# Optimization experiments

Hardware: AMD Instinct MI355X
Metric: run time of the kernel (lower is better)

Reference implementation:

```python
import jax, jax.numpy as jnp
import numpy as np

K = 3        # kernel_size
PAD = 1      # padding
STRIDE = 1   # stride


def conv2d(x, w, stride, pad):
    return jax.lax.conv_general_dilated(
        x, w, (stride, stride), [(pad, pad), (pad, pad)],
        dimension_numbers=('NCHW', 'OIHW', 'NCHW'))


def setup_inputs() -> dict:
    key = jax.random.key(0)
    ks = jax.random.split(key, 6)
    B, C, H, W, O = 8, 64, 64, 64, 128
    N = K * K
    x = jax.random.normal(ks[0], (B, C, H, W), jnp.float32)
    # offset (shift) conv: 2N output channels; small weights so sampled
    # positions deviate a few pixels from the regular grid
    shift_w = jax.random.normal(ks[1], (2 * N, C, 3, 3), jnp.float32) * 0.01
    shift_b = jax.random.normal(ks[2], (2 * N,), jnp.float32) * 0.5
    # modulation conv: N output channels
    mod_w = jax.random.normal(ks[3], (N, C, 3, 3), jnp.float32) * 0.01
    mod_b = jax.random.normal(ks[4], (N,), jnp.float32) * 0.1
    # final conv (bias=False), applied with stride=K on the unfolded map
    conv_w = jax.random.normal(ks[5], (O, C, K, K), jnp.float32) / np.sqrt(C * K * K)
    return {'x': x, 'shift_w': shift_w, 'shift_b': shift_b,
            'mod_w': mod_w, 'mod_b': mod_b, 'conv_w': conv_w}


def reference(x, shift_w, shift_b, mod_w, mod_b, conv_w):
    B, C, H, W = x.shape
    k = conv_w.shape[-1]
    N = k * k
    # offsets and modulation from 3x3 convs on the raw input
    offset = conv2d(x, shift_w, STRIDE, 1) + shift_b[None, :, None, None]   # (B,2N,H,W)
    modulation = jax.nn.sigmoid(conv2d(x, mod_w, STRIDE, 1) + mod_b[None, :, None, None])  # (B,N,H,W)

    xp = jnp.pad(x, ((0, 0), (0, 0), (PAD, PAD), (PAD, PAD)))  # zero padding
    Hp, Wp = xp.shape[2], xp.shape[3]

    # p_n: kernel-relative offsets, ij meshgrid, x-block then y-block -> (2N,)
    r = (k - 1) // 2
    pn_x, pn_y = jnp.meshgrid(jnp.arange(-r, r + 1), jnp.arange(-r, r + 1), indexing='ij')
    pn = jnp.concatenate([pn_x.ravel(), pn_y.ravel()]).astype(x.dtype)
    # p_0: base grid starts at 1 (accounts for padding)
    p0x = jnp.broadcast_to(jnp.arange(1, H * STRIDE + 1, STRIDE, dtype=x.dtype)[:, None], (H, W))
    p0y = jnp.broadcast_to(jnp.arange(1, W * STRIDE + 1, STRIDE, dtype=x.dtype)[None, :], (H, W))
    p0 = jnp.concatenate([jnp.broadcast_to(p0x, (N, H, W)),
                          jnp.broadcast_to(p0y, (N, H, W))], 0)  # (2N,H,W)

    pos = offset + pn[None, :, None, None] + p0[None]            # (B,2N,H,W)
    pos = jnp.transpose(pos, (0, 2, 3, 1))                       # (B,H,W,2N)
    px, py = pos[..., :N], pos[..., N:]

    # NOTE: original clamps to output H/W (not padded dims) -- kept faithfully
    fx, fy = jnp.floor(px), jnp.floor(py)
    lt_x = jnp.clip(fx, 0, H - 1).astype(jnp.int32)
    lt_y = jnp.clip(fy, 0, W - 1).astype(jnp.int32)
    rb_x = jnp.clip(fx + 1, 0, H - 1).astype(jnp.int32)
    rb_y = jnp.clip(fy + 1, 0, W - 1).astype(jnp.int32)
    # original casts clamped position to long -> integer bilinear weights
    p_x = jnp.clip(px, 0, H - 1).astype(jnp.int32)
    p_y = jnp.clip(py, 0, W - 1).astype(jnp.int32)

    g_lt = ((1 + (lt_x - p_x)) * (1 + (lt_y - p_y))).astype(x.dtype)
    g_rb = ((1 - (rb_x - p_x)) * (1 - (rb_y - p_y))).astype(x.dtype)
    g_lb = ((1 + (lt_x - p_x)) * (1 + (rb_y - p_y))).astype(x.dtype)  # lb=(lt_x,rb_y)
    g_rt = ((1 - (rb_x - p_x)) * (1 - (lt_y - p_y))).astype(x.dtype)  # rt=(rb_x,lt_y)

    x_flat = xp.reshape(B, C, Hp * Wp)

    def gather(qx, qy):
        idx = (qx * Wp + qy).reshape(B, 1, -1)                     # (B,1,H*W*N)
        v = jnp.take_along_axis(x_flat, jnp.broadcast_to(idx, (B, C, idx.shape[-1])), axis=-1)
        return v.reshape(B, C, H, W, N)

    x_off = (g_lt[:, None] * gather(lt_x, lt_y)
             + g_rb[:, None] * gather(rb_x, rb_y)
             + g_lb[:, None] * gather(lt_x, rb_y)
             + g_rt[:, None] * gather(rb_x, lt_y))                 # (B,C,H,W,N)

    mod = jnp.transpose(modulation, (0, 2, 3, 1))[:, None]        # (B,1,H,W,N)
    x_off = x_off * mod

    # unfold: out[h*k+a, w*k+b] = x_off[h, w, a*k+b]
    x_off = x_off.reshape(B, C, H, W, k, k).transpose(0, 1, 2, 4, 3, 5).reshape(B, C, H * k, W * k)
    return conv2d(x_off, conv_w, k, 0)                            # (B,O,H,W)
```

## Files before the change

### kernel.cpp

```cpp
#include <hip/hip_runtime.h>
#include <hip/hip_fp16.h>
#include <math.h>


typedef _Float16 half8_t __attribute__((ext_vector_type(8)));
typedef float f32x4 __attribute__((ext_vector_type(4)));

__global__ __launch_bounds__(256) void k_pre(const float* __restrict__ x,
                                             const float* __restrict__ cw,
                                             const float* __restrict__ shift_w,
                                             const float* __restrict__ mod_w,
                                             __half* __restrict__ xTh,
                                             __half* __restrict__ xTl,
                                             __half* __restrict__ xCb,
                                             __half* __restrict__ WtF,
                                             __half* __restrict__ WtSFh,
                                             __half* __restrict__ WtSFl) {
    __shared__ float tile[64][65];
    int bid = blockIdx.x;
    int t = threadIdx.x;
    if (bid < 512) {
        int b = bid >> 6, pt = bid & 63;
        int lane = t & 63, cq = t >> 6;
        const float* xb = x + ((size_t)b << 18);
#pragma unroll
        for (int r = 0; r < 16; ++r) {
            int c = cq * 16 + r;
            tile[c][lane] = xb[((size_t)c << 12) + pt * 64 + lane];
        }
        __syncthreads();
        int p = t >> 2, qc = t & 3;
        __align__(16) _Float16 hh[16];
        __align__(16) _Float16 ll[16];
        __align__(16) _Float16 cb[16];
#pragma unroll
        for (int k = 0; k < 16; ++k) {
            float v0 = tile[qc * 16 + k][p];
            float v1 = (p < 63) ? tile[qc * 16 + k][p + 1] : 0.f;
            _Float16 h = (_Float16)v0;
            hh[k] = h;
            ll[k] = (_Float16)(v0 - (float)h);
            cb[k] = (_Float16)(v0 + 2.f * v1);
        }
        size_t off = ((size_t)b << 18) + (size_t)(pt * 64 + p) * 64 + qc * 16;
        ((uint4*)(xTh + off))[0] = ((uint4*)hh)[0];
        ((uint4*)(xTh + off))[1] = ((uint4*)hh)[1];
        ((uint4*)(xTl + off))[0] = ((uint4*)ll)[0];
        ((uint4*)(xTl + off))[1] = ((uint4*)ll)[1];
        ((uint4*)(xCb + off))[0] = ((uint4*)cb)[0];
        ((uint4*)(xCb + off))[1] = ((uint4*)cb)[1];
    } else {
        int u = (bid - 512) * 256 + t;
        if (u < 73728) {
            int e = u & 7, l = (u >> 3) & 63, ks = (u >> 9) & 1;
            int g = (u >> 10) & 3, w = (u >> 12) & 1, n = u >> 13;
            int o = w * 64 + g * 16 + (l & 15);
            int c = ks * 32 + (l >> 4) * 8 + e;
            WtF[u] = __float2half_rn(cw[(o * 64 + c) * 9 + n]);
        } else {
            int q = u - 73728;
            if (q < 18432) {
                int e = q & 7, l = (q >> 3) & 63, nf = (q >> 9) & 1;
                int chf = (q >> 10) & 1, tap = q >> 11;
                int ch = nf * 16 + (l & 15);
                int c = chf * 32 + (l >> 4) * 8 + e;
                float wv = 0.f;
                if (ch < 18) wv = shift_w[(ch * 64 + c) * 9 + tap];
                else if (ch < 27) wv = mod_w[((ch - 18) * 64 + c) * 9 + tap];
                _Float16 h = (_Float16)wv;
                _Float16 lo = (_Float16)(wv - (float)h);
                WtSFh[q] = *(__half*)&h;
                WtSFl[q] = *(__half*)&lo;
            }
        }
    }
}

__global__ __launch_bounds__(512, 2) void k_fused(
    const __half* __restrict__ xTh, const __half* __restrict__ xTl,
    const __half* __restrict__ xCb, const __half* __restrict__ WtF,
    const __half* __restrict__ WtSFh, const __half* __restrict__ WtSFl,
    const float* __restrict__ shift_b, const float* __restrict__ mod_b,
    float* __restrict__ out) {
    __shared__ __align__(16) unsigned char arena[50688];
    __shared__ float Cw[2][4][16][36];
    __shared__ uint4 recA[9][64];

    int t = threadIdx.x;
    int l = t & 63;
    int w = t >> 6;
    int l15 = l & 15, lhi = l >> 4;

    int bid = blockIdx.x;
    int bk = (bid & 7) * 64 + (bid >> 3);
    int b = bk >> 6;
    int row = bk & 63;

    const __half* xbh = xTh + ((size_t)b << 18);
    const __half* xbl = xTl + ((size_t)b << 18);
    const __half* xbc = xCb + ((size_t)b << 18);

#pragma unroll
    for (int rr = 0; rr < 7; ++rr) {
        int d = rr * 512 + t;
        if (d < 3168) {
            int bufl = d >= 1584 ? 1 : 0;
            int dd = d - bufl * 1584;
            int s = dd >> 3, cb8 = dd & 7;
            int r = s / 66, j = s - r * 66;
            int grow = row + r - 1;
            int gcol = j - 1;
            uint4 v = make_uint4(0u, 0u, 0u, 0u);
            if ((unsigned)grow < 64u && (unsigned)gcol < 64u) {
                const __half* src = (bufl ? xbl : xbh) +
                                    ((size_t)((grow << 6) + gcol) << 6) + (cb8 << 3);
                v = *(const uint4*)src;
            }
            int dst = bufl * 25344 + s * 128 + ((cb8 << 4) ^ ((s & 7) << 4));
            *(uint4*)&arena[dst] = v;
        }
    }
    __syncthreads();

    {
        int wp = w >> 1, wh = w & 1;
        f32x4 accA[2];
        accA[0] = (f32x4){0.f, 0.f, 0.f, 0.f};
        accA[1] = (f32x4){0.f, 0.f, 0.f, 0.f};
#pragma unroll
        for (int tr = 0; tr < 3; ++tr)
#pragma unroll
            for (int tc = 0; tc < 3; ++tc) {
                int tap = tr * 3 + tc;
                int j = wp * 16 + l15 + tc;
                int s = tr * 66 + j;
                int cbyte = (wh << 6) + (lhi << 4);
                int addr = s * 128 + (cbyte ^ ((s & 7) << 4));
                half8_t Ah = *(const half8_t*)&arena[addr];
                half8_t Al = *(const half8_t*)&arena[25344 + addr];
#pragma unroll
                for (int nf = 0; nf < 2; ++nf) {
                    int fo = ((((tap << 1) + wh) << 1) + nf) << 9;
                    half8_t Bh = *(const half8_t*)(WtSFh + fo + (l << 3));
                    half8_t Bl = *(const half8_t*)(WtSFl + fo + (l << 3));
                    accA[nf] = __builtin_amdgcn_mfma_f32_16x16x32_f16(Ah, Bh, accA[nf], 0, 0, 0);
                    accA[nf] = __builtin_amdgcn_mfma_f32_16x16x32_f16(Ah, Bl, accA[nf], 0, 0, 0);
                    accA[nf] = __builtin_amdgcn_mfma_f32_16x16x32_f16(Al, Bh, accA[nf], 0, 0, 0);
                }
            }
#pragma unroll
        for (int nf = 0; nf < 2; ++nf)
#pragma unroll
            for (int v4 = 0; v4 < 4; ++v4)
                Cw[wh][wp][(lhi << 2) + v4][nf * 16 + l15] = accA[nf][v4];
    }
    __syncthreads();

#pragma unroll
    for (int jj0 = 0; jj0 < 2; ++jj0) {
        int rid = jj0 * 512 + t;
        if (rid < 576) {
            int p = rid & 63;
            int n = rid >> 6;
            int wp = p >> 4, pp = p & 15;
            float sx = Cw[0][wp][pp][n] + Cw[1][wp][pp][n];
            float sy = Cw[0][wp][pp][9 + n] + Cw[1][wp][pp][9 + n];
            float sm = Cw[0][wp][pp][18 + n] + Cw[1][wp][pp][18 + n];

            float px = ((sx + shift_b[n]) + (float)(n / 3 - 1)) + (float)(row + 1);
            float py = ((sy + shift_b[9 + n]) + (float)(n % 3 - 1)) + (float)(p + 1);
            float mod = 1.f / (1.f + expf(-(sm + mod_b[n])));

            float fx = floorf(px), fy = floorf(py);
            int ltx = (int)fminf(fmaxf(fx, 0.f), 63.f);
            int lty = (int)fminf(fmaxf(fy, 0.f), 63.f);
            int rbx = (int)fminf(fmaxf(fx + 1.f, 0.f), 63.f);
            int rby = (int)fminf(fmaxf(fy + 1.f, 0.f), 63.f);
            int pxi = (int)fminf(fmaxf(px, 0.f), 63.f);
            int pyi = (int)fminf(fmaxf(py, 0.f), 63.f);

            int g_lt = (1 + ltx - pxi) * (1 + lty - pyi);
            int g_rb = (1 - rbx + pxi) * (1 - rby + pyi);
            int g_lb = (1 + ltx - pxi) * (1 + rby - pyi);
            int g_rt = (1 - rbx + pxi) * (1 - lty + pyi);

            bool simple = (ltx == pxi) && (lty == pyi) && (rbx == pxi + 1) &&
                          (rby == pyi + 1) && (ltx >= 1) && (lty >= 1);

            int qxa[4] = {ltx, rbx, ltx, rbx};
            int qya[4] = {lty, rby, rby, lty};
            int gga[4] = {g_lt, g_rb, g_lb, g_rt};
            unsigned w0 = 0, w1 = 0;
#pragma unroll
            for (int jq = 0; jq < 4; ++jq) {
                bool valid = (qxa[jq] >= 1) && (qya[jq] >= 1);
                unsigned idx = valid ? (unsigned)((qxa[jq] - 1) * 64 + (qya[jq] - 1)) : 0u;
                unsigned gc = valid ? (unsigned)gga[jq] : 0u;
                if (jq < 2) w0 |= idx << (12 * jq); else w1 |= idx << (12 * (jq - 2));
                w0 |= gc << (24 + 2 * jq);
            }
            if (simple) w1 |= 0x80000000u;
            recA[n][p] = make_uint4(w0, w1, __float_as_uint(mod), 0u);
        }
    }
    __syncthreads();

    int wm = w >> 1, wn = w & 1;
    int mA = t >> 3, cg = t & 7;

    f32x4 acc[4];
#pragma unroll
    for (int g = 0; g < 4; ++g) acc[g] = (f32x4){0.f, 0.f, 0.f, 0.f};

    for (int n = 0; n < 9; ++n) {
        int sl = n & 1;
        {
            const uint4* wsrc = (const uint4*)(WtF + n * 8192);
            uint4* wdst = (uint4*)&arena[16384 + (sl << 14)];
            wdst[t] = wsrc[t];
            wdst[512 + t] = wsrc[512 + t];
        }

        {
            uint4 rc = recA[n][mA];
            float mod = __uint_as_float(rc.z);
            __align__(16) __half2 a2[4];
            if (rc.y >> 31) {
                int idx = (int)(rc.x & 0xFFF);
                uint4 v = *(const uint4*)(xbc + (idx << 6) + (cg << 3));
                __half mh = __float2half_rn(mod);
                __half2 mm(mh, mh);
                const __half2* vv = (const __half2*)&v;
                a2[0] = __hmul2(mm, vv[0]);
                a2[1] = __hmul2(mm, vv[1]);
                a2[2] = __hmul2(mm, vv[2]);
                a2[3] = __hmul2(mm, vv[3]);
            } else {
                a2[0] = __half2(0, 0); a2[1] = __half2(0, 0);
                a2[2] = __half2(0, 0); a2[3] = __half2(0, 0);
#pragma unroll
                for (int jq = 0; jq < 4; ++jq) {
                    int id = (int)((jq < 2 ? (rc.x >> (12 * jq))
                                           : (rc.y >> (12 * (jq - 2)))) & 0xFFF);
                    float wf = (float)((rc.x >> (24 + 2 * jq)) & 3) * mod;
                    __half2 wh2 = __half2(__float2half_rn(wf), __float2half_rn(wf));
                    uint4 v = *(const uint4*)(xbh + (id << 6) + (cg << 3));
                    const __half2* vv = (const __half2*)&v;
                    a2[0] = __hfma2(wh2, vv[0], a2[0]);
                    a2[1] = __hfma2(wh2, vv[1], a2[1]);
                    a2[2] = __hfma2(wh2, vv[2], a2[2]);
                    a2[3] = __hfma2(wh2, vv[3], a2[3]);
                }
            }
            *(uint4*)&arena[(sl << 13) | (mA << 7) | ((cg ^ (mA & 7)) << 4)] =
                *(uint4*)a2;
        }
        __syncthreads();

        const unsigned char* wsl = &arena[16384 + (sl << 14)];
#pragma unroll
        for (int ks = 0; ks < 2; ++ks) {
            int rowa = wm * 16 + l15;
            int gr = (ks * 4 + lhi) ^ (rowa & 7);
            half8_t Af = *(const half8_t*)&arena[(sl << 13) | (rowa << 7) | (gr << 4)];
#pragma unroll
            for (int g = 0; g < 4; ++g) {
                half8_t Bf = *(const half8_t*)&wsl[((((wn << 2) + g) << 1) + ks) * 1024 +
                                                   (l << 4)];
                acc[g] = __builtin_amdgcn_mfma_f32_16x16x32_f16(Af, Bf, acc[g], 0, 0, 0);
            }
        }
    }

    __syncthreads();
    float* Ep = (float*)arena;
#pragma unroll
    for (int g = 0; g < 4; ++g) {
        int o_loc = (wn << 6) + (g << 4) + l15;
#pragma unroll
        for (int v4 = 0; v4 < 4; ++v4)
            Ep[o_loc * 65 + (wm << 4) + (lhi << 2) + v4] = acc[g][v4];
    }
    __syncthreads();
    {
        float* ob = out + ((size_t)b << 19);
        int prow = row << 6;
#pragma unroll
        for (int r = 0; r < 4; ++r) {
            int o_loc = (r << 5) + (t >> 4);
            int mseg = t & 15;
            float4 fa;
            fa.x = Ep[o_loc * 65 + mseg * 4 + 0];
            fa.y = Ep[o_loc * 65 + mseg * 4 + 1];
            fa.z = Ep[o_loc * 65 + mseg * 4 + 2];
            fa.w = Ep[o_loc * 65 + mseg * 4 + 3];
            float* dst = ob + (((size_t)o_loc) << 12) + prow + mseg * 4;
            *(float4*)dst = fa;
        }
    }
}

extern "C" void kernel_launch(void* const* d_in, const int* in_sizes, int n_in,
                              void* d_out, int out_size, void* d_ws, size_t ws_size,
                              hipStream_t stream) {
    const float* x = (const float*)d_in[0];
    const float* shift_w = (const float*)d_in[1];
    const float* shift_b = (const float*)d_in[2];
    const float* mod_w = (const float*)d_in[3];
    const float* mod_b = (const float*)d_in[4];
    const float* conv_w = (const float*)d_in[5];
    float* out = (float*)d_out;

    char* ws = (char*)d_ws;
    __half* xTh = (__half*)ws;
    __half* xTl = (__half*)(ws + 4194304);
    __half* xCb = (__half*)(ws + 8388608);
    __half* WtF = (__half*)(ws + 12582912);
    __half* WtSFh = (__half*)(ws + 12730368);
    __half* WtSFl = (__half*)(ws + 12767232);

    k_pre<<<dim3(872), dim3(256), 0, stream>>>(x, conv_w, shift_w, mod_w,
                                               xTh, xTl, xCb, WtF, WtSFh, WtSFl);
    k_fused<<<dim3(512), dim3(512), 0, stream>>>(xTh, xTl, xCb, WtF, WtSFh,
                                                 WtSFl, shift_b, mod_b, out);
}
```

Before: 36.45 us.

## Software-pipeline weight and gather loads ahead of MFMA in main loop

Restructures the 9-tap loop into a prologue plus a pipelined body. The next tap's weights and gathered input values are loaded into registers before the current tap's MFMAs are issued, then written to the alternate LDS slot afterwards. This hides global and gather latency behind matrix compute and needs only one barrier per iteration. The cost is more live registers, which may lower occupancy.

```diff
diff --git a/kernel.cpp b/kernel.cpp
--- a/kernel.cpp
+++ b/kernel.cpp
@@ -212,25 +212,96 @@
 #pragma unroll
     for (int g = 0; g < 4; ++g) acc[g] = (f32x4){0.f, 0.f, 0.f, 0.f};
 
+    {
+        const uint4* wsrc = (const uint4*)WtF;
+        uint4* wdst = (uint4*)&arena[16384];
+        wdst[t] = wsrc[t];
+        wdst[512 + t] = wsrc[512 + t];
+
+        uint4 rc = recA[0][mA];
+        float mod = __uint_as_float(rc.z);
+        __align__(16) __half2 a2[4];
+        if (rc.y >> 31) {
+            int idx = (int)(rc.x & 0xFFF);
+            uint4 v = *(const uint4*)(xbc + (idx << 6) + (cg << 3));
+            __half mh = __float2half_rn(mod);
+            __half2 mm(mh, mh);
+            const __half2* vv = (const __half2*)&v;
+            a2[0] = __hmul2(mm, vv[0]);
+            a2[1] = __hmul2(mm, vv[1]);
+            a2[2] = __hmul2(mm, vv[2]);
+            a2[3] = __hmul2(mm, vv[3]);
+        } else {
+            a2[0] = __half2(0, 0); a2[1] = __half2(0, 0);
+            a2[2] = __half2(0, 0); a2[3] = __half2(0, 0);
+#pragma unroll
+            for (int jq = 0; jq < 4; ++jq) {
+                int id = (int)((jq < 2 ? (rc.x >> (12 * jq))
+                                       : (rc.y >> (12 * (jq - 2)))) & 0xFFF);
+                float wf = (float)((rc.x >> (24 + 2 * jq)) & 3) * mod;
+                __half2 wh2 = __half2(__float2half_rn(wf), __float2half_rn(wf));
+                uint4 v = *(const uint4*)(xbh + (id << 6) + (cg << 3));
+                const __half2* vv = (const __half2*)&v;
+                a2[0] = __hfma2(wh2, vv[0], a2[0]);
+                a2[1] = __hfma2(wh2, vv[1], a2[1]);
+                a2[2] = __hfma2(wh2, vv[2], a2[2]);
+                a2[3] = __hfma2(wh2, vv[3], a2[3]);
+            }
+        }
+        *(uint4*)&arena[(mA << 7) | ((cg ^ (mA & 7)) << 4)] = *(uint4*)a2;
+    }
+    __syncthreads();
+
     for (int n = 0; n < 9; ++n) {
         int sl = n & 1;
+
+        uint4 wv0, wv1, rcN;
+        uint4 gr0, gr1, gr2, gr3;
+        bool simpleN = false;
+        if (n < 8) {
+            const uint4* wsrc = (const uint4*)(WtF + (n + 1) * 8192);
+            wv0 = wsrc[t];
+            wv1 = wsrc[512 + t];
+            rcN = recA[n + 1][mA];
+            simpleN = (rcN.y >> 31) != 0u;
+            if (simpleN) {
+                gr0 = *(const uint4*)(xbc + ((int)(rcN.x & 0xFFF) << 6) + (cg << 3));
+            } else {
+                gr0 = *(const uint4*)(xbh + ((int)(rcN.x & 0xFFF) << 6) + (cg << 3));
+                gr1 = *(const uint4*)(xbh + ((int)((rcN.x >> 12) & 0xFFF) << 6) + (cg << 3));
+                gr2 = *(const uint4*)(xbh + ((int)(rcN.y & 0xFFF) << 6) + (cg << 3));
+                gr3 = *(const uint4*)(xbh + ((int)((rcN.y >> 12) & 0xFFF) << 6) + (cg << 3));
+            }
+        }
+
         {
-            const uint4* wsrc = (const uint4*)(WtF + n * 8192);
-            uint4* wdst = (uint4*)&arena[16384 + (sl << 14)];
-            wdst[t] = wsrc[t];
-            wdst[512 + t] = wsrc[512 + t];
-        }
-
-        {
-            uint4 rc = recA[n][mA];
-            float mod = __uint_as_float(rc.z);
+            const unsigned char* wsl = &arena[16384 + (sl << 14)];
+#pragma unroll
+            for (int ks = 0; ks < 2; ++ks) {
+                int rowa = wm * 16 + l15;
+                int gr = (ks * 4 + lhi) ^ (rowa & 7);
+                half8_t Af = *(const half8_t*)&arena[(sl << 13) | (rowa << 7) | (gr << 4)];
+#pragma unroll
+                for (int g = 0; g < 4; ++g) {
+                    half8_t Bf = *(const half8_t*)&wsl[((((wn << 2) + g) << 1) + ks) * 1024 +
+                                                       (l << 4)];
+                    acc[g] = __builtin_amdgcn_mfma_f32_16x16x32_f16(Af, Bf, acc[g], 0, 0, 0);
+                }
+            }
+        }
+
+        if (n < 8) {
+            int s2 = sl ^ 1;
+            uint4* wdst = (uint4*)&arena[16384 + (s2 << 14)];
+            wdst[t] = wv0;
+            wdst[512 + t] = wv1;
+
+            float mod = __uint_as_float(rcN.z);
             __align__(16) __half2 a2[4];
-            if (rc.y >> 31) {
-                int idx = (int)(rc.x & 0xFFF);
-                uint4 v = *(const uint4*)(xbc + (idx << 6) + (cg << 3));
+            if (simpleN) {
                 __half mh = __float2half_rn(mod);
                 __half2 mm(mh, mh);
-                const __half2* vv = (const __half2*)&v;
+                const __half2* vv = (const __half2*)&gr0;
                 a2[0] = __hmul2(mm, vv[0]);
                 a2[1] = __hmul2(mm, vv[1]);
                 a2[2] = __hmul2(mm, vv[2]);
@@ -238,41 +309,24 @@
             } else {
                 a2[0] = __half2(0, 0); a2[1] = __half2(0, 0);
                 a2[2] = __half2(0, 0); a2[3] = __half2(0, 0);
+                const uint4* grs[4] = {&gr0, &gr1, &gr2, &gr3};
 #pragma unroll
                 for (int jq = 0; jq < 4; ++jq) {
-                    int id = (int)((jq < 2 ? (rc.x >> (12 * jq))
-                                           : (rc.y >> (12 * (jq - 2)))) & 0xFFF);
-                    float wf = (float)((rc.x >> (24 + 2 * jq)) & 3) * mod;
+                    float wf = (float)((rcN.x >> (24 + 2 * jq)) & 3) * mod;
                     __half2 wh2 = __half2(__float2half_rn(wf), __float2half_rn(wf));
-                    uint4 v = *(const uint4*)(xbh + (id << 6) + (cg << 3));
-                    const __half2* vv = (const __half2*)&v;
+                    const __half2* vv = (const __half2*)grs[jq];
                     a2[0] = __hfma2(wh2, vv[0], a2[0]);
                     a2[1] = __hfma2(wh2, vv[1], a2[1]);
                     a2[2] = __hfma2(wh2, vv[2], a2[2]);
                     a2[3] = __hfma2(wh2, vv[3], a2[3]);
                 }
             }
-            *(uint4*)&arena[(sl << 13) | (mA << 7) | ((cg ^ (mA & 7)) << 4)] =
+            *(uint4*)&arena[(s2 << 13) | (mA << 7) | ((cg ^ (mA & 7)) << 4)] =
                 *(uint4*)a2;
         }
         __syncthreads();
-
-        const unsigned char* wsl = &arena[16384 + (sl << 14)];
-#pragma unroll
-        for (int ks = 0; ks < 2; ++ks) {
-            int rowa = wm * 16 + l15;
-            int gr = (ks * 4 + lhi) ^ (rowa & 7);
-            half8_t Af = *(const half8_t*)&arena[(sl << 13) | (rowa << 7) | (gr << 4)];
-#pragma unroll
-            for (int g = 0; g < 4; ++g) {
-                half8_t Bf = *(const half8_t*)&wsl[((((wn << 2) + g) << 1) + ks) * 1024 +
-                                                   (l << 4)];
-                acc[g] = __builtin_amdgcn_mfma_f32_16x16x32_f16(Af, Bf, acc[g], 0, 0, 0);
-            }
-        }
-    }
-
-    __syncthreads();
+    }
+
     float* Ep = (float*)arena;
 #pragma unroll
     for (int g = 0; g < 4; ++g) {
```

Result: faster. 34.85 us (-4.4%).

## Software-pipeline gather and weight loads two stages ahead in fused deformable conv

Applied to the files above, without the earlier changes.

Restructures the main tap loop to issue global gathers and weight loads two iterations ahead into registers, writing the next LDS slab after the MFMA compute of the current slab, with one barrier per iteration instead of an implicit load-then-compute serialization. Also splits the offset-conv MFMA accumulation into three independent accumulators to break the dependency chain. Raises launch bounds to 4 blocks per SM-equivalent, which forces a lower register budget while the prefetch buffers add register pressure, risking spills. The goal is to hide global gather latency behind matrix math.

```diff
diff --git a/kernel.cpp b/kernel.cpp
--- a/kernel.cpp
+++ b/kernel.cpp
@@ -76,7 +76,36 @@
     }
 }
 
-__global__ __launch_bounds__(512, 2) void k_fused(
+__device__ __forceinline__ void combine_frag(uint4 rc, bool simple, float mod,
+                                             const uint4& g0, const uint4& g1,
+                                             const uint4& g2, const uint4& g3,
+                                             __half2* a2) {
+    if (simple) {
+        __half mh = __float2half_rn(mod);
+        __half2 mm(mh, mh);
+        const __half2* vv = (const __half2*)&g0;
+        a2[0] = __hmul2(mm, vv[0]);
+        a2[1] = __hmul2(mm, vv[1]);
+        a2[2] = __hmul2(mm, vv[2]);
+        a2[3] = __hmul2(mm, vv[3]);
+    } else {
+        a2[0] = __half2(0, 0); a2[1] = __half2(0, 0);
+        a2[2] = __half2(0, 0); a2[3] = __half2(0, 0);
+        const uint4* grs[4] = {&g0, &g1, &g2, &g3};
+#pragma unroll
+        for (int jq = 0; jq < 4; ++jq) {
+            float wf = (float)((rc.x >> (24 + 2 * jq)) & 3) * mod;
+            __half2 wh2 = __half2(__float2half_rn(wf), __float2half_rn(wf));
+            const __half2* vv = (const __half2*)grs[jq];
+            a2[0] = __hfma2(wh2, vv[0], a2[0]);
+            a2[1] = __hfma2(wh2, vv[1], a2[1]);
+            a2[2] = __hfma2(wh2, vv[2], a2[2]);
+            a2[3] = __hfma2(wh2, vv[3], a2[3]);
+        }
+    }
+}
+
+__global__ __launch_bounds__(512, 4) void k_fused(
     const __half* __restrict__ xTh, const __half* __restrict__ xTl,
     const __half* __restrict__ xCb, const __half* __restrict__ WtF,
     const __half* __restrict__ WtSFh, const __half* __restrict__ WtSFl,
@@ -124,9 +153,13 @@
 
     {
         int wp = w >> 1, wh = w & 1;
-        f32x4 accA[2];
-        accA[0] = (f32x4){0.f, 0.f, 0.f, 0.f};
-        accA[1] = (f32x4){0.f, 0.f, 0.f, 0.f};
+        f32x4 aP[2], aQ[2], aR[2];
+#pragma unroll
+        for (int nf = 0; nf < 2; ++nf) {
+            aP[nf] = (f32x4){0.f, 0.f, 0.f, 0.f};
+            aQ[nf] = (f32x4){0.f, 0.f, 0.f, 0.f};
+            aR[nf] = (f32x4){0.f, 0.f, 0.f, 0.f};
+        }
 #pragma unroll
         for (int tr = 0; tr < 3; ++tr)
 #pragma unroll
@@ -143,16 +176,17 @@
                     int fo = ((((tap << 1) + wh) << 1) + nf) << 9;
                     half8_t Bh = *(const half8_t*)(WtSFh + fo + (l << 3));
                     half8_t Bl = *(const half8_t*)(WtSFl + fo + (l << 3));
-                    accA[nf] = __builtin_amdgcn_mfma_f32_16x16x32_f16(Ah, Bh, accA[nf], 0, 0, 0);
-                    accA[nf] = __builtin_amdgcn_mfma_f32_16x16x32_f16(Ah, Bl, accA[nf], 0, 0, 0);
-                    accA[nf] = __builtin_amdgcn_mfma_f32_16x16x32_f16(Al, Bh, accA[nf], 0, 0, 0);
+                    aP[nf] = __builtin_amdgcn_mfma_f32_16x16x32_f16(Ah, Bh, aP[nf], 0, 0, 0);
+                    aQ[nf] = __builtin_amdgcn_mfma_f32_16x16x32_f16(Ah, Bl, aQ[nf], 0, 0, 0);
+                    aR[nf] = __builtin_amdgcn_mfma_f32_16x16x32_f16(Al, Bh, aR[nf], 0, 0, 0);
                 }
             }
 #pragma unroll
         for (int nf = 0; nf < 2; ++nf)
 #pragma unroll
             for (int v4 = 0; v4 < 4; ++v4)
-                Cw[wh][wp][(lhi << 2) + v4][nf * 16 + l15] = accA[nf][v4];
+                Cw[wh][wp][(lhi << 2) + v4][nf * 16 + l15] =
+                    (aP[nf][v4] + aQ[nf][v4]) + aR[nf][v4];
     }
     __syncthreads();
 
@@ -212,67 +246,80 @@
 #pragma unroll
     for (int g = 0; g < 4; ++g) acc[g] = (f32x4){0.f, 0.f, 0.f, 0.f};
 
+#define ISSUE(W0, W1, RC, SMP, G0, G1, G2, G3, nn)                             \
+    {                                                                          \
+        const uint4* wsrc_ = (const uint4*)(WtF + (nn) * 8192);                \
+        W0 = wsrc_[t];                                                         \
+        W1 = wsrc_[512 + t];                                                   \
+        RC = recA[nn][mA];                                                     \
+        SMP = (RC.y >> 31) != 0u;                                              \
+        if (SMP) {                                                             \
+            G0 = *(const uint4*)(xbc + ((int)(RC.x & 0xFFF) << 6) + (cg << 3));\
+        } else {                                                               \
+            G0 = *(const uint4*)(xbh + ((int)(RC.x & 0xFFF) << 6) + (cg << 3));\
+            G1 = *(const uint4*)(xbh + ((int)((RC.x >> 12) & 0xFFF) << 6) + (cg << 3)); \
+            G2 = *(const uint4*)(xbh + ((int)(RC.y & 0xFFF) << 6) + (cg << 3));\
+            G3 = *(const uint4*)(xbh + ((int)((RC.y >> 12) & 0xFFF) << 6) + (cg << 3)); \
+        }                                                                      \
+    }
+
+#define WRITE_SLAB(W0, W1, RC, SMP, G0, G1, G2, G3, slot)                      \
+    {                                                                          \
+        uint4* wdst_ = (uint4*)&arena[16384 + ((slot) << 14)];                 \
+        wdst_[t] = W0;                                                         \
+        wdst_[512 + t] = W1;                                                   \
+        __align__(16) __half2 a2_[4];                                          \
+        combine_frag(RC, SMP, __uint_as_float(RC.z), G0, G1, G2, G3, a2_);     \
+        *(uint4*)&arena[((slot) << 13) | (mA << 7) | ((cg ^ (mA & 7)) << 4)] = \
+            *(uint4*)a2_;                                                      \
+    }
+
+    uint4 wA0, wA1, rcA_, gA0, gA1, gA2, gA3;
+    uint4 wB0, wB1, rcB_, gB0, gB1, gB2, gB3;
+    bool smA = false, smB = false;
+
+    ISSUE(wA0, wA1, rcA_, smA, gA0, gA1, gA2, gA3, 0);
+    WRITE_SLAB(wA0, wA1, rcA_, smA, gA0, gA1, gA2, gA3, 0);
+    ISSUE(wA0, wA1, rcA_, smA, gA0, gA1, gA2, gA3, 1);
+    __syncthreads();
+
+#pragma unroll
     for (int n = 0; n < 9; ++n) {
         int sl = n & 1;
+
+        if (n < 7) {
+            ISSUE(wB0, wB1, rcB_, smB, gB0, gB1, gB2, gB3, n + 2);
+        }
+
         {
-            const uint4* wsrc = (const uint4*)(WtF + n * 8192);
-            uint4* wdst = (uint4*)&arena[16384 + (sl << 14)];
-            wdst[t] = wsrc[t];
-            wdst[512 + t] = wsrc[512 + t];
-        }
-
-        {
-            uint4 rc = recA[n][mA];
-            float mod = __uint_as_float(rc.z);
-            __align__(16) __half2 a2[4];
-            if (rc.y >> 31) {
-                int idx = (int)(rc.x & 0xFFF);
-                uint4 v = *(const uint4*)(xbc + (idx << 6) + (cg << 3));
-                __half mh = __float2half_rn(mod);
-                __half2 mm(mh, mh);
-                const __half2* vv = (const __half2*)&v;
-                a2[0] = __hmul2(mm, vv[0]);
-                a2[1] = __hmul2(mm, vv[1]);
-                a2[2] = __hmul2(mm, vv[2]);
-                a2[3] = __hmul2(mm, vv[3]);
-            } else {
-                a2[0] = __half2(0, 0); a2[1] = __half2(0, 0);
-                a2[2] = __half2(0, 0); a2[3] = __half2(0, 0);
-#pragma unroll
-                for (int jq = 0; jq < 4; ++jq) {
-                    int id = (int)((jq < 2 ? (rc.x >> (12 * jq))
-                                           : (rc.y >> (12 * (jq - 2)))) & 0xFFF);
-                    float wf = (float)((rc.x >> (24 + 2 * jq)) & 3) * mod;
-                    __half2 wh2 = __half2(__float2half_rn(wf), __float2half_rn(wf));
-                    uint4 v = *(const uint4*)(xbh + (id << 6) + (cg << 3));
-                    const __half2* vv = (const __half2*)&v;
-                    a2[0] = __hfma2(wh2, vv[0], a2[0]);
-                    a2[1] = __hfma2(wh2, vv[1], a2[1]);
-                    a2[2] = __hfma2(wh2, vv[2], a2[2]);
-                    a2[3] = __hfma2(wh2, vv[3], a2[3]);
+            const unsigned char* wsl = &arena[16384 + (sl << 14)];
+#pragma unroll
+            for (int ks = 0; ks < 2; ++ks) {
+                int rowa = wm * 16 + l15;
+                int gr = (ks * 4 + lhi) ^ (rowa & 7);
+                half8_t Af = *(const half8_t*)&arena[(sl << 13) | (rowa << 7) | (gr << 4)];
+#pragma unroll
+                for (int g = 0; g < 4; ++g) {
+                    half8_t Bf = *(const half8_t*)&wsl[((((wn << 2) + g) << 1) + ks) * 1024 +
+                                                       (l << 4)];
+                    acc[g] = __builtin_amdgcn_mfma_f32_16x16x32_f16(Af, Bf, acc[g], 0, 0, 0);
                 }
             }
-            *(uint4*)&arena[(sl << 13) | (mA << 7) | ((cg ^ (mA & 7)) << 4)] =
-                *(uint4*)a2;
+        }
+
+        if (n < 8) {
+            WRITE_SLAB(wA0, wA1, rcA_, smA, gA0, gA1, gA2, gA3, sl ^ 1);
+        }
+
+        if (n < 7) {
+            wA0 = wB0; wA1 = wB1; rcA_ = rcB_; smA = smB;
+            gA0 = gB0; gA1 = gB1; gA2 = gB2; gA3 = gB3;
         }
         __syncthreads();
-
-        const unsigned char* wsl = &arena[16384 + (sl << 14)];
-#pragma unroll
-        for (int ks = 0; ks < 2; ++ks) {
-            int rowa = wm * 16 + l15;
-            int gr = (ks * 4 + lhi) ^ (rowa & 7);
-            half8_t Af = *(const half8_t*)&arena[(sl << 13) | (rowa << 7) | (gr << 4)];
-#pragma unroll
-            for (int g = 0; g < 4; ++g) {
-                half8_t Bf = *(const half8_t*)&wsl[((((wn << 2) + g) << 1) + ks) * 1024 +
-                                                   (l << 4)];
-                acc[g] = __builtin_amdgcn_mfma_f32_16x16x32_f16(Af, Bf, acc[g], 0, 0, 0);
-            }
-        }
-    }
-
-    __syncthreads();
+    }
+#undef ISSUE
+#undef WRITE_SLAB
+
     float* Ep = (float*)arena;
 #pragma unroll
     for (int g = 0; g < 4; ++g) {
```

Result: faster. 35.23 us (-3.3%).

## Gather A fragments directly into registers and software-pipeline weight loads

Applied to the files above, without the earlier changes.

The bilinear gather now writes MFMA A-fragments straight into registers instead of staging them through shared memory. Each thread gathers two 8-half chunks for its own MFMA row, so pixels are gathered redundantly across the two wn warps. Weight tiles and A-fragments for the next tap are prefetched into registers while the current tap's MFMAs run, then weights are stored into the alternate LDS buffer. This aims to hide global-memory latency behind compute and drop the LDS round trip for A. The cost is more register pressure and duplicated gather loads.

```diff
diff --git a/kernel.cpp b/kernel.cpp
--- a/kernel.cpp
+++ b/kernel.cpp
@@ -76,6 +76,54 @@
     }
 }
 
+__device__ __forceinline__ void gather_afrag(const __half* __restrict__ xbc,
+                                             const __half* __restrict__ xbh,
+                                             int coff, uint4 rc,
+                                             half8_t& A0, half8_t& A1) {
+    float modf = __uint_as_float(rc.z);
+    if (rc.y >> 31) {
+        const __half* p0 = xbc + (((int)(rc.x & 0xFFF)) << 6) + coff;
+        uint4 L0 = *(const uint4*)p0;
+        uint4 L1 = *(const uint4*)(p0 + 32);
+        __half mh = __float2half_rn(modf);
+        __half2 mm(mh, mh);
+        const __half2* v0 = (const __half2*)&L0;
+        const __half2* v1 = (const __half2*)&L1;
+        __align__(16) __half2 a0[4], a1[4];
+#pragma unroll
+        for (int j = 0; j < 4; ++j) {
+            a0[j] = __hmul2(mm, v0[j]);
+            a1[j] = __hmul2(mm, v1[j]);
+        }
+        A0 = *(half8_t*)a0;
+        A1 = *(half8_t*)a1;
+    } else {
+        __align__(16) __half2 a0[4], a1[4];
+#pragma unroll
+        for (int j = 0; j < 4; ++j) { a0[j] = __half2(0, 0); a1[j] = __half2(0, 0); }
+        int ids[4] = {(int)(rc.x & 0xFFF), (int)((rc.x >> 12) & 0xFFF),
+                      (int)(rc.y & 0xFFF), (int)((rc.y >> 12) & 0xFFF)};
+#pragma unroll
+        for (int jq = 0; jq < 4; ++jq) {
+            const __half* ph = xbh + (ids[jq] << 6) + coff;
+            uint4 H0 = *(const uint4*)ph;
+            uint4 H1 = *(const uint4*)(ph + 32);
+            float wf = (float)((rc.x >> (24 + 2 * jq)) & 3) * modf;
+            __half wh = __float2half_rn(wf);
+            __half2 w2(wh, wh);
+            const __half2* u0 = (const __half2*)&H0;
+            const __half2* u1 = (const __half2*)&H1;
+#pragma unroll
+            for (int j = 0; j < 4; ++j) {
+                a0[j] = __hfma2(w2, u0[j], a0[j]);
+                a1[j] = __hfma2(w2, u1[j], a1[j]);
+            }
+        }
+        A0 = *(half8_t*)a0;
+        A1 = *(half8_t*)a1;
+    }
+}
+
 __global__ __launch_bounds__(512, 2) void k_fused(
     const __half* __restrict__ xTh, const __half* __restrict__ xTl,
     const __half* __restrict__ xCb, const __half* __restrict__ WtF,
@@ -206,73 +254,61 @@
     __syncthreads();
 
     int wm = w >> 1, wn = w & 1;
-    int mA = t >> 3, cg = t & 7;
+    int pixA = (wm << 4) + l15;
+    int coff = lhi << 3;
 
     f32x4 acc[4];
 #pragma unroll
     for (int g = 0; g < 4; ++g) acc[g] = (f32x4){0.f, 0.f, 0.f, 0.f};
+
+    half8_t AfC0, AfC1, AfN0, AfN1;
+
+    {
+        const uint4* wsrc = (const uint4*)WtF;
+        uint4* wdst = (uint4*)&arena[16384];
+        wdst[t] = wsrc[t];
+        wdst[512 + t] = wsrc[512 + t];
+        gather_afrag(xbc, xbh, coff, recA[0][pixA], AfC0, AfC1);
+    }
+    __syncthreads();
 
     for (int n = 0; n < 9; ++n) {
         int sl = n & 1;
+
+        uint4 wv0, wv1;
+        if (n < 8) {
+            const uint4* wsrc = (const uint4*)(WtF + (n + 1) * 8192);
+            wv0 = wsrc[t];
+            wv1 = wsrc[512 + t];
+            gather_afrag(xbc, xbh, coff, recA[n + 1][pixA], AfN0, AfN1);
+        }
+
+        __builtin_amdgcn_s_setprio(1);
         {
-            const uint4* wsrc = (const uint4*)(WtF + n * 8192);
-            uint4* wdst = (uint4*)&arena[16384 + (sl << 14)];
-            wdst[t] = wsrc[t];
-            wdst[512 + t] = wsrc[512 + t];
-        }
-
-        {
-            uint4 rc = recA[n][mA];
-            float mod = __uint_as_float(rc.z);
-            __align__(16) __half2 a2[4];
-            if (rc.y >> 31) {
-                int idx = (int)(rc.x & 0xFFF);
-                uint4 v = *(const uint4*)(xbc + (idx << 6) + (cg << 3));
-                __half mh = __float2half_rn(mod);
-                __half2 mm(mh, mh);
-                const __half2* vv = (const __half2*)&v;
-                a2[0] = __hmul2(mm, vv[0]);
-                a2[1] = __hmul2(mm, vv[1]);
-                a2[2] = __hmul2(mm, vv[2]);
-                a2[3] = __hmul2(mm, vv[3]);
-            } else {
-                a2[0] = __half2(0, 0); a2[1] = __half2(0, 0);
-                a2[2] = __half2(0, 0); a2[3] = __half2(0, 0);
-#pragma unroll
-                for (int jq = 0; jq < 4; ++jq) {
-                    int id = (int)((jq < 2 ? (rc.x >> (12 * jq))
-                                           : (rc.y >> (12 * (jq - 2)))) & 0xFFF);
-                    float wf = (float)((rc.x >> (24 + 2 * jq)) & 3) * mod;
-                    __half2 wh2 = __half2(__float2half_rn(wf), __float2half_rn(wf));
-                    uint4 v = *(const uint4*)(xbh + (id << 6) + (cg << 3));
-                    const __half2* vv = (const __half2*)&v;
-                    a2[0] = __hfma2(wh2, vv[0], a2[0]);
-                    a2[1] = __hfma2(wh2, vv[1], a2[1]);
-                    a2[2] = __hfma2(wh2, vv[2], a2[2]);
-                    a2[3] = __hfma2(wh2, vv[3], a2[3]);
-                }
-            }
-            *(uint4*)&arena[(sl << 13) | (mA << 7) | ((cg ^ (mA & 7)) << 4)] =
-                *(uint4*)a2;
+            const unsigned char* wsl = &arena[16384 + (sl << 14)];
+#pragma unroll
+            for (int g = 0; g < 4; ++g) {
+                half8_t Bf0 = *(const half8_t*)&wsl[((((wn << 2) + g) << 1) + 0) * 1024 + (l << 4)];
+                acc[g] = __builtin_amdgcn_mfma_f32_16x16x32_f16(AfC0, Bf0, acc[g], 0, 0, 0);
+            }
+#pragma unroll
+            for (int g = 0; g < 4; ++g) {
+                half8_t Bf1 = *(const half8_t*)&wsl[((((wn << 2) + g) << 1) + 1) * 1024 + (l << 4)];
+                acc[g] = __builtin_amdgcn_mfma_f32_16x16x32_f16(AfC1, Bf1, acc[g], 0, 0, 0);
+            }
+        }
+        __builtin_amdgcn_s_setprio(0);
+
+        if (n < 8) {
+            uint4* wdst = (uint4*)&arena[16384 + ((sl ^ 1) << 14)];
+            wdst[t] = wv0;
+            wdst[512 + t] = wv1;
+            AfC0 = AfN0;
+            AfC1 = AfN1;
         }
         __syncthreads();
-
-        const unsigned char* wsl = &arena[16384 + (sl << 14)];
-#pragma unroll
-        for (int ks = 0; ks < 2; ++ks) {
-            int rowa = wm * 16 + l15;
-            int gr = (ks * 4 + lhi) ^ (rowa & 7);
-            half8_t Af = *(const half8_t*)&arena[(sl << 13) | (rowa << 7) | (gr << 4)];
-#pragma unroll
-            for (int g = 0; g < 4; ++g) {
-                half8_t Bf = *(const half8_t*)&wsl[((((wn << 2) + g) << 1) + ks) * 1024 +
-                                                   (l << 4)];
-                acc[g] = __builtin_amdgcn_mfma_f32_16x16x32_f16(Af, Bf, acc[g], 0, 0, 0);
-            }
-        }
-    }
-
-    __syncthreads();
+    }
+
     float* Ep = (float*)arena;
 #pragma unroll
     for (int g = 0; g < 4; ++g) {
```

Measured after the change: 48.17 us. 1.32x slower.
